# Kernel optimization log

Hardware: AMD Instinct MI355X
Metric: run time of the kernel (lower is better)

Reference implementation:

```python
import jax, jax.numpy as jnp
import numpy as np

B, N, E = 4, 25000, 1600000
NODE_DIM, EMBED = 64, 64
NUM = B * N


def setup_inputs() -> dict:
    key = jax.random.key(0)
    ks = jax.random.split(key, 12)
    p = lambda k, s: jax.random.normal(k, s, jnp.float32) * 0.05
    z = lambda s: jnp.zeros(s, jnp.float32)
    return {
        "node_feat": jax.random.normal(ks[0], (B, N, NODE_DIM), jnp.float32),
        "src": jax.random.randint(ks[1], (E,), 0, NUM),
        "dst": jax.random.randint(ks[2], (E,), 0, NUM),
        "edge_weight": jax.random.uniform(ks[3], (E,), jnp.float32),
        "h": z((NUM, EMBED)),
        "W_cz": p(ks[4], (NODE_DIM, EMBED)), "b_cz": z((EMBED,)),
        "W_cr": p(ks[5], (NODE_DIM, EMBED)), "b_cr": z((EMBED,)),
        "W_ch": p(ks[6], (NODE_DIM, EMBED)), "b_ch": z((EMBED,)),
        "W_lz": p(ks[7], (2 * EMBED, EMBED)), "b_lz": z((EMBED,)),
        "W_lr": p(ks[8], (2 * EMBED, EMBED)), "b_lr": z((EMBED,)),
        "W_lh": p(ks[9], (2 * EMBED, EMBED)), "b_lh": z((EMBED,)),
        "W_head": p(ks[10], (EMBED, 1)), "b_head": z((1,)),
    }


def gcn_conv(x, W, b, src, dst, ew):
    # PyG GCNConv: self-loops (fill=1) + symmetric normalization, then linear.
    n = x.shape[0]
    loop = jnp.arange(n)
    s = jnp.concatenate([src, loop])
    d = jnp.concatenate([dst, loop])
    w = jnp.concatenate([ew, jnp.ones((n,), x.dtype)])
    deg = jax.ops.segment_sum(w, d, num_segments=n)
    dinv = jnp.where(deg > 0, jax.lax.rsqrt(deg), 0.0)
    norm = dinv[s] * w * dinv[d]                      # [E+n]
    xw = x @ W                                        # [n, EMBED]
    out = jax.ops.segment_sum(xw[s] * norm[:, None], d, num_segments=n)
    return out + b


def tgcn_cell(x, h, src, dst, ew,
              W_cz, b_cz, W_cr, b_cr, W_ch, b_ch,
              W_lz, b_lz, W_lr, b_lr, W_lh, b_lh):
    Z = jax.nn.sigmoid(
        jnp.concatenate([gcn_conv(x, W_cz, b_cz, src, dst, ew), h], axis=1) @ W_lz + b_lz)
    R = jax.nn.sigmoid(
        jnp.concatenate([gcn_conv(x, W_cr, b_cr, src, dst, ew), h], axis=1) @ W_lr + b_lr)
    H_tilde = jnp.tanh(
        jnp.concatenate([gcn_conv(x, W_ch, b_ch, src, dst, ew), h * R], axis=1) @ W_lh + b_lh)
    return Z * h + (1.0 - Z) * H_tilde


def reference(node_feat, src, dst, edge_weight, h,
              W_cz, b_cz, W_cr, b_cr, W_ch, b_ch,
              W_lz, b_lz, W_lr, b_lr, W_lh, b_lh,
              W_head, b_head):
    Bv, Nv, _ = node_feat.shape
    x = node_feat.reshape(Bv * Nv, -1)
    h0 = tgcn_cell(x, h, src, dst, edge_weight,
                   W_cz, b_cz, W_cr, b_cr, W_ch, b_ch,
                   W_lz, b_lz, W_lr, b_lr, W_lh, b_lh)
    z = jax.nn.relu(h0)
    z = (z @ W_head + b_head).reshape(Bv, Nv, -1)
    return (z, h0)
```

## Files before the change

### kernel.cpp

```cpp
#include <hip/hip_runtime.h>
#include <hip/hip_fp16.h>
#include <stdint.h>

typedef unsigned long long u64;
typedef _Float16 half8 __attribute__((ext_vector_type(8)));
typedef float f32x4 __attribute__((ext_vector_type(4)));

#define EPB 6144
#define CAPC 5440

__device__ __forceinline__ float sigm(float x) { return 1.0f / (1.0f + __expf(-x)); }
__device__ __forceinline__ float tanhfast(float x) { return 1.0f - 2.0f / (__expf(2.0f * x) + 1.0f); }
__device__ __forceinline__ int rli(int v, int k) { return __builtin_amdgcn_readlane(v, k); }
__device__ __forceinline__ float rlf(float v, int k) {
    return __int_as_float(__builtin_amdgcn_readlane(__float_as_int(v), k));
}

__global__ void k_weights(const float* __restrict__ Wcz, const float* __restrict__ bcz,
                          const float* __restrict__ Wcr, const float* __restrict__ bcr,
                          const float* __restrict__ Wch, const float* __restrict__ bch,
                          const float* __restrict__ Wlz, const float* __restrict__ blz,
                          const float* __restrict__ Wlr, const float* __restrict__ blr,
                          const float* __restrict__ Wlh, const float* __restrict__ blh,
                          __half* __restrict__ B1f, __half* __restrict__ B2f,
                          float* __restrict__ bias, int* __restrict__ cursor) {
    int tid = blockIdx.x * 256 + threadIdx.x;
    if (tid < 1024) cursor[tid] = 0;
    if (tid < 24576) {
        int k = tid / 192, nc = tid % 192;
        int g = nc >> 6, j = nc & 63;
        const float* Wc = (g == 0) ? Wcz : (g == 1) ? Wcr : Wch;
        const float* Wl = (g == 0) ? Wlz : (g == 1) ? Wlr : Wlh;
        float v;
        if (k < 64) {
            float acc = 0.f;
            for (int m = 0; m < 64; m++) acc += Wc[k * 64 + m] * Wl[m * 64 + j];
            v = acc;
        } else {
            v = (g < 2) ? Wl[k * 64 + j] : 0.f;
        }
        int kt = k >> 5, nt = nc >> 4;
        int lane = (((k >> 3) & 3) << 4) | (nc & 15);
        B1f[(((kt * 12 + nt) * 64 + lane) << 3) + (k & 7)] = (__half)v;
    } else if (tid < 24576 + 4096) {
        int t = tid - 24576;
        int k = t >> 6, nc = t & 63;
        float v = Wlh[(64 + k) * 64 + nc];
        int kt = k >> 5, nt = nc >> 4;
        int lane = (((k >> 3) & 3) << 4) | (nc & 15);
        B2f[(((kt * 4 + nt) * 64 + lane) << 3) + (k & 7)] = (__half)v;
    } else if (tid < 24576 + 4096 + 192) {
        int t = tid - 24576 - 4096;
        int g = t >> 6, j = t & 63;
        const float* bc = (g == 0) ? bcz : (g == 1) ? bcr : bch;
        const float* Wl = (g == 0) ? Wlz : (g == 1) ? Wlr : Wlh;
        const float* bl = (g == 0) ? blz : (g == 1) ? blr : blh;
        float acc = bl[j];
        for (int m = 0; m < 64; m++) acc += bc[m] * Wl[m * 64 + j];
        bias[t] = acc;
    }
}

__global__ void k_init(const float4* __restrict__ x4, const float4* __restrict__ h4,
                       __half* __restrict__ xh, __half* __restrict__ aggh, int nq) {
    int i = blockIdx.x * blockDim.x + threadIdx.x;
    if (i < nq) {
        float4 xv = x4[i];
        float4 hv = h4[i];
        int elem = i * 4;
        int node = elem >> 6, c = elem & 63;
        __half2* xo = (__half2*)(xh + elem);
        xo[0] = __floats2half2_rn(xv.x, xv.y);
        xo[1] = __floats2half2_rn(xv.z, xv.w);
        __half2* ho = (__half2*)(aggh + (((size_t)node) << 7) + 64 + c);
        ho[0] = __floats2half2_rn(hv.x, hv.y);
        ho[1] = __floats2half2_rn(hv.z, hv.w);
    }
}

__global__ void __launch_bounds__(512) k_bin(const int* __restrict__ src, const int* __restrict__ dst,
                                             const float* __restrict__ ew,
                                             int* __restrict__ cursor, u64* __restrict__ binned,
                                             int E, int R) {
    __shared__ u64 recs[EPB];
    __shared__ int hist[512];
    __shared__ int loff[512];
    __shared__ int curL[512];
    __shared__ int gbase[512];

    int tid = threadIdx.x;
    hist[tid] = 0;
    __syncthreads();

    int base = blockIdx.x * EPB;
    int cntE = min(EPB, E - base);

    u64 myrec[12];
    int myr[12];
#pragma unroll
    for (int j = 0; j < 12; j++) {
        int idx = tid + j * 512;
        if (idx < cntE) {
            int e = base + idx;
            int d = dst[e], s = src[e];
            float w = ew[e];
            int r = d >> 8;
            myr[j] = r;
            myrec[j] = (u64)((unsigned)s | ((unsigned)(d & 255) << 17)) | ((u64)__float_as_uint(w) << 32);
            atomicAdd(&hist[r], 1);
        } else myr[j] = -1;
    }
    __syncthreads();

    if (tid < 64) {
        int sums[8], tot = 0;
#pragma unroll
        for (int q = 0; q < 8; q++) { sums[q] = hist[tid * 8 + q]; tot += sums[q]; }
        int scan = tot;
#pragma unroll
        for (int o = 1; o < 64; o <<= 1) {
            int v = __shfl_up(scan, o);
            if (tid >= o) scan += v;
        }
        int run = scan - tot;
#pragma unroll
        for (int q = 0; q < 8; q++) { loff[tid * 8 + q] = run; run += sums[q]; }
    }
    curL[tid] = 0;
    if (tid < R) {
        int hcnt = hist[tid];
        if (hcnt > 0) gbase[tid] = tid * CAPC + atomicAdd(&cursor[tid], hcnt);
    }
    __syncthreads();

#pragma unroll
    for (int j = 0; j < 12; j++) {
        if (myr[j] >= 0) {
            int p = atomicAdd(&curL[myr[j]], 1);
            recs[loff[myr[j]] + p] = myrec[j];
        }
    }
    __syncthreads();

    int wave = tid >> 6, lane = tid & 63;
    for (int r = wave; r < R; r += 8) {
        int len = hist[r];
        if (!len) continue;
        int gb = gbase[r], lo = loff[r];
        int capEnd = (r + 1) * CAPC;
        for (int i = lane; i < len; i += 64)
            if (gb + i < capEnd) binned[(size_t)(gb + i)] = recs[lo + i];
    }
}

__global__ void __launch_bounds__(512) k_sort(const int* __restrict__ cursor,
                                              u64* __restrict__ binned,
                                              float* __restrict__ dinv,
                                              int* __restrict__ off_g, int* __restrict__ len_g,
                                              int n) {
    __shared__ u64 srt[CAPC];
    __shared__ int hist[256];
    __shared__ int noff[256];
    __shared__ int cur[256];
    __shared__ float degw[256];

    int r = blockIdx.x, tid = threadIdx.x;
    if (tid < 256) { hist[tid] = 0; degw[tid] = 0.f; }
    __syncthreads();

    int cnt = min(cursor[r], CAPC);
    u64* B = binned + (size_t)r * CAPC;

    for (int i = tid; i < cnt; i += 512) {
        u64 m = B[i];
        int dl = ((unsigned)m >> 17) & 255;
        atomicAdd(&hist[dl], 1);
        atomicAdd(&degw[dl], __uint_as_float((unsigned)(m >> 32)));
    }
    __syncthreads();

    if (tid < 64) {
        int s0 = hist[tid * 4], s1 = hist[tid * 4 + 1], s2 = hist[tid * 4 + 2], s3 = hist[tid * 4 + 3];
        int tot = s0 + s1 + s2 + s3;
        int scan = tot;
#pragma unroll
        for (int o = 1; o < 64; o <<= 1) {
            int v = __shfl_up(scan, o);
            if (tid >= o) scan += v;
        }
        int run = scan - tot;
        noff[tid * 4] = run; run += s0;
        noff[tid * 4 + 1] = run; run += s1;
        noff[tid * 4 + 2] = run; run += s2;
        noff[tid * 4 + 3] = run;
    }
    __syncthreads();

    if (tid < 256) {
        int node = r * 256 + tid;
        if (node < n) {
            dinv[node] = rsqrtf(1.0f + degw[tid]);
            off_g[node] = r * CAPC + noff[tid];
            len_g[node] = hist[tid];
        }
        cur[tid] = noff[tid];
    }
    __syncthreads();

    for (int i = tid; i < cnt; i += 512) {
        u64 m = B[i];
        int dl = ((unsigned)m >> 17) & 255;
        int p = atomicAdd(&cur[dl], 1);
        srt[p] = (u64)((unsigned)m & 0x1FFFF) | (m & 0xFFFFFFFF00000000ULL);
    }
    __syncthreads();

    for (int i = tid; i < cnt; i += 512) B[i] = srt[i];
}

__global__ void __launch_bounds__(256) k_gather(const int* __restrict__ off_g, const int* __restrict__ len_g,
                                                const u64* __restrict__ csr, const float* __restrict__ dinv,
                                                const __half* __restrict__ xh,
                                                __half* __restrict__ aggh, int n) {
    int lane = threadIdx.x & 63;
    int wid = __builtin_amdgcn_readfirstlane(threadIdx.x >> 6);
    int d = blockIdx.x * 4 + wid;
    if (d >= n) return;
    int o0 = off_g[d], L = len_g[d];
    float dd = dinv[d];
    float acc0 = dd * dd * (float)xh[((size_t)d << 6) + lane];
    float acc1 = 0.f, acc2 = 0.f, acc3 = 0.f;

    for (int base = 0; base < L; base += 64) {
        int c = min(64, L - base);
        u64 m = (lane < c) ? csr[(size_t)o0 + base + lane] : 0;
        int s_l = (int)(unsigned)m;
        float ew_l = __uint_as_float((unsigned)(m >> 32));
        float nrm_l = (lane < c) ? ew_l * dinv[s_l] * dd : 0.f;
        int k = 0;
        for (; k + 4 <= c; k += 4) {
            int s0 = rli(s_l, k), s1 = rli(s_l, k + 1), s2 = rli(s_l, k + 2), s3 = rli(s_l, k + 3);
            float n0 = rlf(nrm_l, k), n1 = rlf(nrm_l, k + 1), n2 = rlf(nrm_l, k + 2), n3 = rlf(nrm_l, k + 3);
            acc0 += n0 * (float)xh[((size_t)s0 << 6) + lane];
            acc1 += n1 * (float)xh[((size_t)s1 << 6) + lane];
            acc2 += n2 * (float)xh[((size_t)s2 << 6) + lane];
            acc3 += n3 * (float)xh[((size_t)s3 << 6) + lane];
        }
        for (; k < c; k++) {
            int s0 = rli(s_l, k);
            float n0 = rlf(nrm_l, k);
            acc0 += n0 * (float)xh[((size_t)s0 << 6) + lane];
        }
    }
    aggh[((size_t)d << 7) + lane] = (__half)((acc0 + acc1) + (acc2 + acc3));
}

__global__ void __launch_bounds__(256, 2) k_node(
        const __half* __restrict__ aggh,
        const __half* __restrict__ B1f_g, const __half* __restrict__ B2f_g,
        const float* __restrict__ bias_g, const float* __restrict__ Whead,
        const float* __restrict__ bhead,
        float* __restrict__ out_head, float* __restrict__ out_h, int n) {

    __shared__ __half B1s[24576];
    __shared__ __half B2s[4096];
    __shared__ float biasS[192];
    __shared__ float whS[64];
    __shared__ __half hrb[4][16 * 72];

    int tid = threadIdx.x;
    {
        const uint4* s1 = (const uint4*)B1f_g; uint4* d1 = (uint4*)B1s;
        for (int i = tid; i < 3072; i += 256) d1[i] = s1[i];
        const uint4* s2 = (const uint4*)B2f_g; uint4* d2 = (uint4*)B2s;
        for (int i = tid; i < 512; i += 256) d2[i] = s2[i];
        if (tid < 192) biasS[tid] = bias_g[tid];
        if (tid < 64) whS[tid] = Whead[tid];
    }
    __syncthreads();

    int lane = tid & 63;
    int wave = tid >> 6;
    int quad = lane >> 4;
    int l15 = lane & 15;

    float bz4[4], br4[4], bh4[4], wh4[4];
#pragma unroll
    for (int nt = 0; nt < 4; nt++) {
        bz4[nt] = biasS[nt * 16 + l15];
        br4[nt] = biasS[64 + nt * 16 + l15];
        bh4[nt] = biasS[128 + nt * 16 + l15];
        wh4[nt] = whS[nt * 16 + l15];
    }
    float bhv = bhead[0];
    __half* myhr = &hrb[wave][0];
    const half8* B1v = (const half8*)B1s;
    const half8* B2v = (const half8*)B2s;

    int tiles = (n + 63) >> 6;
    for (int t = blockIdx.x; t < tiles; t += gridDim.x) {
        int mbase = t * 64 + wave * 16;
        if (mbase >= n) continue;

        const half8* arow = (const half8*)(aggh + (((size_t)(mbase + l15)) << 7) + (quad << 3));
        half8 a0 = arow[0], a1 = arow[4], a2 = arow[8], a3 = arow[12];

        f32x4 acc[12];
#pragma unroll
        for (int nt = 0; nt < 12; nt++) acc[nt] = (f32x4){0.f, 0.f, 0.f, 0.f};

#pragma unroll
        for (int nt = 0; nt < 12; nt++) {
            acc[nt] = __builtin_amdgcn_mfma_f32_16x16x32_f16(a0, B1v[(0 * 12 + nt) * 64 + lane], acc[nt], 0, 0, 0);
            acc[nt] = __builtin_amdgcn_mfma_f32_16x16x32_f16(a1, B1v[(1 * 12 + nt) * 64 + lane], acc[nt], 0, 0, 0);
            acc[nt] = __builtin_amdgcn_mfma_f32_16x16x32_f16(a2, B1v[(2 * 12 + nt) * 64 + lane], acc[nt], 0, 0, 0);
            acc[nt] = __builtin_amdgcn_mfma_f32_16x16x32_f16(a3, B1v[(3 * 12 + nt) * 64 + lane], acc[nt], 0, 0, 0);
        }

        float hv[4][4];
#pragma unroll
        for (int nt = 0; nt < 4; nt++)
#pragma unroll
            for (int r = 0; r < 4; r++)
                hv[nt][r] = (float)aggh[(((size_t)(mbase + quad * 4 + r)) << 7) + 64 + nt * 16 + l15];

        float Z[4][4];
#pragma unroll
        for (int nt = 0; nt < 4; nt++)
#pragma unroll
            for (int r = 0; r < 4; r++) {
                Z[nt][r] = sigm(acc[nt][r] + bz4[nt]);
                float R = sigm(acc[4 + nt][r] + br4[nt]);
                myhr[(quad * 4 + r) * 72 + nt * 16 + l15] = (__half)(hv[nt][r] * R);
            }
        __builtin_amdgcn_s_waitcnt(0);

        half8 a2f0 = *(const half8*)(myhr + l15 * 72 + quad * 8);
        half8 a2f1 = *(const half8*)(myhr + l15 * 72 + 32 + quad * 8);

#pragma unroll
        for (int nt = 0; nt < 4; nt++) {
            acc[8 + nt] = __builtin_amdgcn_mfma_f32_16x16x32_f16(a2f0, B2v[(0 * 4 + nt) * 64 + lane], acc[8 + nt], 0, 0, 0);
            acc[8 + nt] = __builtin_amdgcn_mfma_f32_16x16x32_f16(a2f1, B2v[(1 * 4 + nt) * 64 + lane], acc[8 + nt], 0, 0, 0);
        }

        float pr0 = 0.f, pr1 = 0.f, pr2 = 0.f, pr3 = 0.f;
#pragma unroll
        for (int nt = 0; nt < 4; nt++) {
#pragma unroll
            for (int r = 0; r < 4; r++) {
                float Ht = tanhfast(acc[8 + nt][r] + bh4[nt]);
                float z = Z[nt][r];
                float hn = z * hv[nt][r] + (1.f - z) * Ht;
                out_h[((size_t)(mbase + quad * 4 + r)) * 64 + nt * 16 + l15] = hn;
                float rv = fmaxf(hn, 0.f) * wh4[nt];
                if (r == 0) pr0 += rv; else if (r == 1) pr1 += rv; else if (r == 2) pr2 += rv; else pr3 += rv;
            }
        }
#pragma unroll
        for (int o = 1; o < 16; o <<= 1) {
            pr0 += __shfl_xor(pr0, o);
            pr1 += __shfl_xor(pr1, o);
            pr2 += __shfl_xor(pr2, o);
            pr3 += __shfl_xor(pr3, o);
        }
        if (l15 == 0) {
            out_head[mbase + quad * 4 + 0] = pr0 + bhv;
            out_head[mbase + quad * 4 + 1] = pr1 + bhv;
            out_head[mbase + quad * 4 + 2] = pr2 + bhv;
            out_head[mbase + quad * 4 + 3] = pr3 + bhv;
        }
    }
}

extern "C" void kernel_launch(void* const* d_in, const int* in_sizes, int n_in,
                              void* d_out, int out_size, void* d_ws, size_t ws_size,
                              hipStream_t stream) {
    const float* x     = (const float*)d_in[0];
    const int*   src   = (const int*)d_in[1];
    const int*   dst   = (const int*)d_in[2];
    const float* ew    = (const float*)d_in[3];
    const float* h     = (const float*)d_in[4];
    const float* Wcz   = (const float*)d_in[5];
    const float* bcz   = (const float*)d_in[6];
    const float* Wcr   = (const float*)d_in[7];
    const float* bcr   = (const float*)d_in[8];
    const float* Wch   = (const float*)d_in[9];
    const float* bch   = (const float*)d_in[10];
    const float* Wlz   = (const float*)d_in[11];
    const float* blz   = (const float*)d_in[12];
    const float* Wlr   = (const float*)d_in[13];
    const float* blr   = (const float*)d_in[14];
    const float* Wlh   = (const float*)d_in[15];
    const float* blh   = (const float*)d_in[16];
    const float* Whead = (const float*)d_in[17];
    const float* bhead = (const float*)d_in[18];

    int E = in_sizes[1];
    int n = in_sizes[4] / 64;
    int R = (n + 255) >> 8;

    __half* aggh = (__half*)d_ws;
    __half* xh   = aggh + (size_t)n * 128;
    u64*   binned = (u64*)(xh + (size_t)n * 64);
    float* dinv  = (float*)(binned + (size_t)R * CAPC);
    int*   off_g = (int*)(dinv + n);
    int*   len_g = off_g + n;
    int*   cursor = len_g + n;
    __half* B1f  = (__half*)(cursor + 1024);
    __half* B2f  = B1f + 24576;
    float* bias  = (float*)(B2f + 4096);

    float* out_head = (float*)d_out;
    float* out_h    = out_head + n;

    int nq = n * 16;
    int nbB = (E + EPB - 1) / EPB;

    k_weights<<<113, 256, 0, stream>>>(Wcz, bcz, Wcr, bcr, Wch, bch,
                                       Wlz, blz, Wlr, blr, Wlh, blh, B1f, B2f, bias, cursor);
    k_init<<<(nq + 255) / 256, 256, 0, stream>>>((const float4*)x, (const float4*)h, xh, aggh, nq);
    k_bin<<<nbB, 512, 0, stream>>>(src, dst, ew, cursor, binned, E, R);
    k_sort<<<R, 512, 0, stream>>>(cursor, binned, dinv, off_g, len_g, n);
    k_gather<<<(n + 3) / 4, 256, 0, stream>>>(off_g, len_g, binned, dinv, xh, aggh, n);
    k_node<<<512, 256, 0, stream>>>(aggh, B1f, B2f, bias, Whead, bhead,
                                    out_head, out_h, n);
}
```

Measured before the change: 259.5 us.

## Prescale node features by dinv in sort kernel and simplify gather normalization

Merges the weight-prep and h-conversion kernels into one launch, and moves the x fp16 conversion into k_sort, where each node's features are prescaled by its dinv. The gather then only multiplies by the edge weight per edge and applies the destination dinv once at the end. This removes the per-edge dinv[src] random load and the separate init launch, and widens the gather unroll to 8 independent loads. In exchange k_sort does extra per-node feature work, and the conversion now sits on the sort kernel's critical path.

```diff
diff --git a/kernel.cpp b/kernel.cpp
--- a/kernel.cpp
+++ b/kernel.cpp
@@ -16,65 +16,62 @@
     return __int_as_float(__builtin_amdgcn_readlane(__float_as_int(v), k));
 }
 
-__global__ void k_weights(const float* __restrict__ Wcz, const float* __restrict__ bcz,
-                          const float* __restrict__ Wcr, const float* __restrict__ bcr,
-                          const float* __restrict__ Wch, const float* __restrict__ bch,
-                          const float* __restrict__ Wlz, const float* __restrict__ blz,
-                          const float* __restrict__ Wlr, const float* __restrict__ blr,
-                          const float* __restrict__ Wlh, const float* __restrict__ blh,
-                          __half* __restrict__ B1f, __half* __restrict__ B2f,
-                          float* __restrict__ bias, int* __restrict__ cursor) {
-    int tid = blockIdx.x * 256 + threadIdx.x;
-    if (tid < 1024) cursor[tid] = 0;
-    if (tid < 24576) {
-        int k = tid / 192, nc = tid % 192;
-        int g = nc >> 6, j = nc & 63;
-        const float* Wc = (g == 0) ? Wcz : (g == 1) ? Wcr : Wch;
-        const float* Wl = (g == 0) ? Wlz : (g == 1) ? Wlr : Wlh;
-        float v;
-        if (k < 64) {
-            float acc = 0.f;
-            for (int m = 0; m < 64; m++) acc += Wc[k * 64 + m] * Wl[m * 64 + j];
-            v = acc;
-        } else {
-            v = (g < 2) ? Wl[k * 64 + j] : 0.f;
-        }
-        int kt = k >> 5, nt = nc >> 4;
-        int lane = (((k >> 3) & 3) << 4) | (nc & 15);
-        B1f[(((kt * 12 + nt) * 64 + lane) << 3) + (k & 7)] = (__half)v;
-    } else if (tid < 24576 + 4096) {
-        int t = tid - 24576;
-        int k = t >> 6, nc = t & 63;
-        float v = Wlh[(64 + k) * 64 + nc];
-        int kt = k >> 5, nt = nc >> 4;
-        int lane = (((k >> 3) & 3) << 4) | (nc & 15);
-        B2f[(((kt * 4 + nt) * 64 + lane) << 3) + (k & 7)] = (__half)v;
-    } else if (tid < 24576 + 4096 + 192) {
-        int t = tid - 24576 - 4096;
-        int g = t >> 6, j = t & 63;
-        const float* bc = (g == 0) ? bcz : (g == 1) ? bcr : bch;
-        const float* Wl = (g == 0) ? Wlz : (g == 1) ? Wlr : Wlh;
-        const float* bl = (g == 0) ? blz : (g == 1) ? blr : blh;
-        float acc = bl[j];
-        for (int m = 0; m < 64; m++) acc += bc[m] * Wl[m * 64 + j];
-        bias[t] = acc;
-    }
-}
-
-__global__ void k_init(const float4* __restrict__ x4, const float4* __restrict__ h4,
-                       __half* __restrict__ xh, __half* __restrict__ aggh, int nq) {
-    int i = blockIdx.x * blockDim.x + threadIdx.x;
-    if (i < nq) {
-        float4 xv = x4[i];
-        float4 hv = h4[i];
-        int elem = i * 4;
-        int node = elem >> 6, c = elem & 63;
-        __half2* xo = (__half2*)(xh + elem);
-        xo[0] = __floats2half2_rn(xv.x, xv.y);
-        xo[1] = __floats2half2_rn(xv.z, xv.w);
-        __half2* ho = (__half2*)(aggh + (((size_t)node) << 7) + 64 + c);
-        ho[0] = __floats2half2_rn(hv.x, hv.y);
-        ho[1] = __floats2half2_rn(hv.z, hv.w);
+__global__ void k_pre(const float* __restrict__ Wcz, const float* __restrict__ bcz,
+                      const float* __restrict__ Wcr, const float* __restrict__ bcr,
+                      const float* __restrict__ Wch, const float* __restrict__ bch,
+                      const float* __restrict__ Wlz, const float* __restrict__ blz,
+                      const float* __restrict__ Wlr, const float* __restrict__ blr,
+                      const float* __restrict__ Wlh, const float* __restrict__ blh,
+                      const float4* __restrict__ h4, __half* __restrict__ aggh,
+                      __half* __restrict__ B1f, __half* __restrict__ B2f,
+                      float* __restrict__ bias, int* __restrict__ cursor, int hq) {
+    int bid = blockIdx.x;
+    if (bid < 113) {
+        int tid = bid * 256 + threadIdx.x;
+        if (tid < 1024) cursor[tid] = 0;
+        if (tid < 24576) {
+            int k = tid / 192, nc = tid % 192;
+            int g = nc >> 6, j = nc & 63;
+            const float* Wc = (g == 0) ? Wcz : (g == 1) ? Wcr : Wch;
+            const float* Wl = (g == 0) ? Wlz : (g == 1) ? Wlr : Wlh;
+            float v;
+            if (k < 64) {
+                float acc = 0.f;
+                for (int m = 0; m < 64; m++) acc += Wc[k * 64 + m] * Wl[m * 64 + j];
+                v = acc;
+            } else {
+                v = (g < 2) ? Wl[k * 64 + j] : 0.f;
+            }
+            int kt = k >> 5, nt = nc >> 4;
+            int lane = (((k >> 3) & 3) << 4) | (nc & 15);
+            B1f[(((kt * 12 + nt) * 64 + lane) << 3) + (k & 7)] = (__half)v;
+        } else if (tid < 24576 + 4096) {
+            int t = tid - 24576;
+            int k = t >> 6, nc = t & 63;
+            float v = Wlh[(64 + k) * 64 + nc];
+            int kt = k >> 5, nt = nc >> 4;
+            int lane = (((k >> 3) & 3) << 4) | (nc & 15);
+            B2f[(((kt * 4 + nt) * 64 + lane) << 3) + (k & 7)] = (__half)v;
+        } else if (tid < 24576 + 4096 + 192) {
+            int t = tid - 24576 - 4096;
+            int g = t >> 6, j = t & 63;
+            const float* bc = (g == 0) ? bcz : (g == 1) ? bcr : bch;
+            const float* Wl = (g == 0) ? Wlz : (g == 1) ? Wlr : Wlh;
+            const float* bl = (g == 0) ? blz : (g == 1) ? blr : blh;
+            float acc = bl[j];
+            for (int m = 0; m < 64; m++) acc += bc[m] * Wl[m * 64 + j];
+            bias[t] = acc;
+        }
+    } else {
+        int i = (bid - 113) * 256 + threadIdx.x;
+        if (i < hq) {
+            float4 hv = h4[i];
+            int elem = i * 4;
+            int node = elem >> 6, c = elem & 63;
+            __half2* ho = (__half2*)(aggh + (((size_t)node) << 7) + 64 + c);
+            ho[0] = __floats2half2_rn(hv.x, hv.y);
+            ho[1] = __floats2half2_rn(hv.z, hv.w);
+        }
     }
 }
 
@@ -155,7 +152,9 @@
 
 __global__ void __launch_bounds__(512) k_sort(const int* __restrict__ cursor,
                                               u64* __restrict__ binned,
+                                              const float2* __restrict__ x2,
                                               float* __restrict__ dinv,
+                                              __half2* __restrict__ xs2,
                                               int* __restrict__ off_g, int* __restrict__ len_g,
                                               int n) {
     __shared__ u64 srt[CAPC];
@@ -198,12 +197,14 @@
 
     if (tid < 256) {
         int node = r * 256 + tid;
+        float dv = rsqrtf(1.0f + degw[tid]);
         if (node < n) {
-            dinv[node] = rsqrtf(1.0f + degw[tid]);
+            dinv[node] = dv;
             off_g[node] = r * CAPC + noff[tid];
             len_g[node] = hist[tid];
         }
         cur[tid] = noff[tid];
+        degw[tid] = dv;
     }
     __syncthreads();
 
@@ -216,11 +217,21 @@
     __syncthreads();
 
     for (int i = tid; i < cnt; i += 512) B[i] = srt[i];
+    int nbase = r * 256;
+    for (int i = tid; i < 256 * 32; i += 512) {
+        int nl = i >> 5, cp = i & 31;
+        int node = nbase + nl;
+        if (node < n) {
+            float2 xv = x2[((size_t)node << 5) + cp];
+            float dv = degw[nl];
+            xs2[((size_t)node << 5) + cp] = __floats2half2_rn(dv * xv.x, dv * xv.y);
+        }
+    }
 }
 
 __global__ void __launch_bounds__(256) k_gather(const int* __restrict__ off_g, const int* __restrict__ len_g,
                                                 const u64* __restrict__ csr, const float* __restrict__ dinv,
-                                                const __half* __restrict__ xh,
+                                                const __half* __restrict__ xs,
                                                 __half* __restrict__ aggh, int n) {
     int lane = threadIdx.x & 63;
     int wid = __builtin_amdgcn_readfirstlane(threadIdx.x >> 6);
@@ -228,31 +239,43 @@
     if (d >= n) return;
     int o0 = off_g[d], L = len_g[d];
     float dd = dinv[d];
-    float acc0 = dd * dd * (float)xh[((size_t)d << 6) + lane];
-    float acc1 = 0.f, acc2 = 0.f, acc3 = 0.f;
+    float a0, a1 = 0.f, a2 = 0.f, a3 = 0.f, a4 = 0.f, a5 = 0.f, a6 = 0.f, a7 = 0.f;
+    a0 = (float)xs[((size_t)d << 6) + lane];
 
     for (int base = 0; base < L; base += 64) {
         int c = min(64, L - base);
-        u64 m = (lane < c) ? csr[(size_t)o0 + base + lane] : 0;
-        int s_l = (int)(unsigned)m;
-        float ew_l = __uint_as_float((unsigned)(m >> 32));
-        float nrm_l = (lane < c) ? ew_l * dinv[s_l] * dd : 0.f;
+        u64 m = (lane < c) ? csr[(size_t)(o0 + base) + lane] : 0;
+        int s_l = (unsigned)m & 0x1FFFF;
+        float w_l = __uint_as_float((unsigned)(m >> 32));
         int k = 0;
+        for (; k + 8 <= c; k += 8) {
+            int ss[8]; float ww[8], xr[8];
+#pragma unroll
+            for (int j = 0; j < 8; j++) { ss[j] = rli(s_l, k + j); ww[j] = rlf(w_l, k + j); }
+#pragma unroll
+            for (int j = 0; j < 8; j++) xr[j] = (float)xs[((size_t)ss[j] << 6) + lane];
+            a0 = fmaf(ww[0], xr[0], a0); a1 = fmaf(ww[1], xr[1], a1);
+            a2 = fmaf(ww[2], xr[2], a2); a3 = fmaf(ww[3], xr[3], a3);
+            a4 = fmaf(ww[4], xr[4], a4); a5 = fmaf(ww[5], xr[5], a5);
+            a6 = fmaf(ww[6], xr[6], a6); a7 = fmaf(ww[7], xr[7], a7);
+        }
         for (; k + 4 <= c; k += 4) {
-            int s0 = rli(s_l, k), s1 = rli(s_l, k + 1), s2 = rli(s_l, k + 2), s3 = rli(s_l, k + 3);
-            float n0 = rlf(nrm_l, k), n1 = rlf(nrm_l, k + 1), n2 = rlf(nrm_l, k + 2), n3 = rlf(nrm_l, k + 3);
-            acc0 += n0 * (float)xh[((size_t)s0 << 6) + lane];
-            acc1 += n1 * (float)xh[((size_t)s1 << 6) + lane];
-            acc2 += n2 * (float)xh[((size_t)s2 << 6) + lane];
-            acc3 += n3 * (float)xh[((size_t)s3 << 6) + lane];
+            int ss[4]; float ww[4], xr[4];
+#pragma unroll
+            for (int j = 0; j < 4; j++) { ss[j] = rli(s_l, k + j); ww[j] = rlf(w_l, k + j); }
+#pragma unroll
+            for (int j = 0; j < 4; j++) xr[j] = (float)xs[((size_t)ss[j] << 6) + lane];
+            a0 = fmaf(ww[0], xr[0], a0); a1 = fmaf(ww[1], xr[1], a1);
+            a2 = fmaf(ww[2], xr[2], a2); a3 = fmaf(ww[3], xr[3], a3);
         }
         for (; k < c; k++) {
             int s0 = rli(s_l, k);
-            float n0 = rlf(nrm_l, k);
-            acc0 += n0 * (float)xh[((size_t)s0 << 6) + lane];
-        }
-    }
-    aggh[((size_t)d << 7) + lane] = (__half)((acc0 + acc1) + (acc2 + acc3));
+            float w0 = rlf(w_l, k);
+            a0 = fmaf(w0, (float)xs[((size_t)s0 << 6) + lane], a0);
+        }
+    }
+    float s = ((a0 + a1) + (a2 + a3)) + ((a4 + a5) + (a6 + a7));
+    aggh[((size_t)d << 7) + lane] = (__half)(dd * s);
 }
 
 __global__ void __launch_bounds__(256, 2) k_node(
@@ -401,8 +424,8 @@
     int R = (n + 255) >> 8;
 
     __half* aggh = (__half*)d_ws;
-    __half* xh   = aggh + (size_t)n * 128;
-    u64*   binned = (u64*)(xh + (size_t)n * 64);
+    __half* xs   = aggh + (size_t)n * 128;
+    u64*   binned = (u64*)(xs + (size_t)n * 64);
     float* dinv  = (float*)(binned + (size_t)R * CAPC);
     int*   off_g = (int*)(dinv + n);
     int*   len_g = off_g + n;
@@ -414,15 +437,17 @@
     float* out_head = (float*)d_out;
     float* out_h    = out_head + n;
 
-    int nq = n * 16;
+    int hq = n * 16;
     int nbB = (E + EPB - 1) / EPB;
-
-    k_weights<<<113, 256, 0, stream>>>(Wcz, bcz, Wcr, bcr, Wch, bch,
-                                       Wlz, blz, Wlr, blr, Wlh, blh, B1f, B2f, bias, cursor);
-    k_init<<<(nq + 255) / 256, 256, 0, stream>>>((const float4*)x, (const float4*)h, xh, aggh, nq);
+    int gridPre = 113 + (hq + 255) / 256;
+
+    k_pre<<<gridPre, 256, 0, stream>>>(Wcz, bcz, Wcr, bcr, Wch, bch,
+                                       Wlz, blz, Wlr, blr, Wlh, blh,
+                                       (const float4*)h, aggh, B1f, B2f, bias, cursor, hq);
     k_bin<<<nbB, 512, 0, stream>>>(src, dst, ew, cursor, binned, E, R);
-    k_sort<<<R, 512, 0, stream>>>(cursor, binned, dinv, off_g, len_g, n);
-    k_gather<<<(n + 3) / 4, 256, 0, stream>>>(off_g, len_g, binned, dinv, xh, aggh, n);
+    k_sort<<<R, 512, 0, stream>>>(cursor, binned, (const float2*)x, dinv,
+                                  (__half2*)xs, off_g, len_g, n);
+    k_gather<<<(n + 3) / 4, 256, 0, stream>>>(off_g, len_g, binned, dinv, xs, aggh, n);
     k_node<<<512, 256, 0, stream>>>(aggh, B1f, B2f, bias, Whead, bhead,
                                     out_head, out_h, n);
 }
```

Measured after the change: 253.6 us. 2.3% less time.
